# Performance work log

Measured on AMD Instinct MI355X. Metric: run time of the kernel, lower is better.

## Reference

```python
import jax, jax.numpy as jnp
import numpy as np

MARGIN = 1.0
N, D = 4096, 512
NUM_CLASSES = 64


def setup_inputs() -> dict:
    key = jax.random.key(0)
    k1, k2 = jax.random.split(key)
    inputs = jax.random.normal(k1, (N, D), dtype=jnp.float32)
    targets = jax.random.randint(k2, (N,), 0, NUM_CLASSES, dtype=jnp.int64)
    return {"inputs": inputs, "targets": targets}


def reference(inputs, targets):
    n = inputs.shape[0]
    sq = jnp.sum(inputs * inputs, axis=1)  # [n]
    # squared Euclidean distances, clamped at 0 (matches relu in original)
    d2 = jnp.maximum(sq[:, None] + sq[None, :] - 2.0 * (inputs @ inputs.T), 0.0)
    # safe sqrt (zero entries get 0, matching forward; avoids NaN grads)
    dist = jnp.where(d2 > 0, jnp.sqrt(jnp.where(d2 > 0, d2, 1.0)), 0.0)  # [n,n]

    same = targets[:, None] == targets[None, :]
    eye = jnp.eye(n, dtype=bool)
    pos_mask = same & ~eye          # positives, diagonal excluded
    neg_mask = ~same                # negatives (diagonal is same-label, excluded)

    # per-row sum_k exp(margin - d_ik) over negatives  (replaces per-pair loop)
    neg_sum = jnp.sum(jnp.where(neg_mask, jnp.exp(MARGIN - dist), 0.0), axis=1)  # [n]

    # J_ij = log(neg_sum_i + neg_sum_j) + d_ij for positive pairs
    J = jnp.log(neg_sum[:, None] + neg_sum[None, :]) + dist
    triu_pos = jnp.triu(pos_mask)   # loop iterated over upper-triangular positives
    hinge2 = jnp.where(triu_pos, jax.nn.relu(J) ** 2, 0.0)

    # original divides by count of ALL positive entries (both triangles)
    len_p = jnp.sum(pos_mask).astype(jnp.float32)
    return jnp.sum(hinge2) / len_p
```

## Files before the change

kernel.cpp:

```cpp
#include <hip/hip_runtime.h>
#include <math.h>

#define NN 4096
#define DD 512
#define MARGINF 1.0f
#define NCLS 64
#define MAXM 160
#define TRI (MAXM * (MAXM - 1) / 2)

typedef __attribute__((ext_vector_type(8))) short bf16x8;
typedef __attribute__((ext_vector_type(4))) float f32x4;

#define WS_SQ   0
#define WS_NS   4096
#define WS_LOSS 8192
#define WS_CNT  8256
#define WS_RK   8320
#define WS_MEM  12416
#define WS_XB   32768
#define WS_PD   1081344

__device__ __forceinline__ unsigned short f2bf(float f) {
    unsigned u = __float_as_uint(f);
    u += 0x7fffu + ((u >> 16) & 1u);
    return (unsigned short)(u >> 16);
}

__device__ __forceinline__ void gl_lds16(const void* g, void* l) {
    __builtin_amdgcn_global_load_lds(
        (__attribute__((address_space(1))) unsigned int*)g,
        (__attribute__((address_space(3))) unsigned int*)l,
        16, 0, 0);
}

__global__ __launch_bounds__(256) void prep_kernel(const float* __restrict__ X,
                                                   float* __restrict__ ws) {
    const int wv = threadIdx.x >> 6, lane = threadIdx.x & 63;
    const int row = blockIdx.x * 4 + wv;
    const float4* xr = (const float4*)(X + (size_t)row * DD);
    float4 a = xr[lane], b = xr[lane + 64];
    float s = a.x * a.x + a.y * a.y + a.z * a.z + a.w * a.w
            + b.x * b.x + b.y * b.y + b.z * b.z + b.w * b.w;
#pragma unroll
    for (int off = 32; off; off >>= 1) s += __shfl_down(s, off, 64);
    if (lane == 0) { ws[WS_SQ + row] = s; ws[WS_NS + row] = 0.0f; }
    ushort4 pa = {f2bf(a.x), f2bf(a.y), f2bf(a.z), f2bf(a.w)};
    ushort4 pb = {f2bf(b.x), f2bf(b.y), f2bf(b.z), f2bf(b.w)};
    ushort4* xb = (ushort4*)((unsigned short*)(ws + WS_XB) + (size_t)row * DD);
    xb[lane] = pa;
    xb[lane + 64] = pb;
    if (blockIdx.x == 0) {
        if (threadIdx.x < NCLS) ((int*)(ws + WS_CNT))[threadIdx.x] = 0;
        if (threadIdx.x == 0) ws[WS_LOSS] = 0.0f;
    }
}

__global__ __launch_bounds__(256) void class_build_kernel(const int* __restrict__ tgt,
                                                          float* __restrict__ ws) {
    const int t = blockIdx.x * 256 + threadIdx.x;
    const int c = tgt[t];
    int* counts = (int*)(ws + WS_CNT);
    int* rk  = (int*)(ws + WS_RK);
    int* mem = (int*)(ws + WS_MEM);
    int p = atomicAdd(&counts[c], 1);
    rk[t] = p;
    if (p < MAXM) mem[c * MAXM + p] = t;
}

__global__ __launch_bounds__(256) void negsum_kernel(const int* __restrict__ tgt,
                                                     float* __restrict__ ws) {
    __shared__ unsigned short As[128 * 32];
    __shared__ unsigned short Bs[128 * 32];

    const int bidx = blockIdx.x;
    int bj = (int)((sqrtf(8.0f * (float)bidx + 1.0f) - 1.0f) * 0.5f);
    while (bj * (bj + 1) / 2 > bidx) --bj;
    while ((bj + 1) * (bj + 2) / 2 <= bidx) ++bj;
    const int bi = bidx - bj * (bj + 1) / 2;
    const int i0 = bi * 128, j0 = bj * 128;

    const int tid = threadIdx.x;
    const int w = tid >> 6, lane = tid & 63;
    const int lr = lane >> 2, lc = lane & 3;
    const unsigned short* Xb = (const unsigned short*)(ws + WS_XB);

    const unsigned short* ga0 = Xb + (size_t)(i0 + w * 16 + lr) * DD + lc * 8;
    const unsigned short* ga1 = ga0 + (size_t)64 * DD;
    const unsigned short* gb0 = Xb + (size_t)(j0 + w * 16 + lr) * DD + lc * 8;
    const unsigned short* gb1 = gb0 + (size_t)64 * DD;
    unsigned short* la0 = &As[(w * 16) * 32];
    unsigned short* la1 = &As[(64 + w * 16) * 32];
    unsigned short* lb0 = &Bs[(w * 16) * 32];
    unsigned short* lb1 = &Bs[(64 + w * 16) * 32];

    const int m_ = lane & 15, q = lane >> 4;
    const int wrow = (w >> 1) * 64, wcol = (w & 1) * 64;

    f32x4 acc[4][4] = {};

    for (int k0 = 0; k0 < DD; k0 += 32) {
        __syncthreads();
        gl_lds16(ga0 + k0, la0);
        gl_lds16(ga1 + k0, la1);
        gl_lds16(gb0 + k0, lb0);
        gl_lds16(gb1 + k0, lb1);
        __syncthreads();
        bf16x8 af[4], bf[4];
#pragma unroll
        for (int u = 0; u < 4; ++u)
            af[u] = *(const bf16x8*)&As[(wrow + u * 16 + m_) * 32 + q * 8];
#pragma unroll
        for (int v = 0; v < 4; ++v)
            bf[v] = *(const bf16x8*)&Bs[(wcol + v * 16 + m_) * 32 + q * 8];
#pragma unroll
        for (int u = 0; u < 4; ++u)
#pragma unroll
            for (int v = 0; v < 4; ++v)
                acc[u][v] = __builtin_amdgcn_mfma_f32_16x16x32_bf16(
                    af[u], bf[v], acc[u][v], 0, 0, 0);
    }

    const float* sq = ws + WS_SQ;
    float* ns = ws + WS_NS;
    const int* rk = (const int*)(ws + WS_RK);
    float* posd = ws + WS_PD;
    float sjv[4]; int tjv[4], jv[4];
#pragma unroll
    for (int v = 0; v < 4; ++v) {
        int j = j0 + wcol + v * 16 + m_;
        jv[v] = j;
        sjv[v] = sq[j];
        tjv[v] = tgt[j];
    }
    float colp[4] = {0.0f, 0.0f, 0.0f, 0.0f};
#pragma unroll
    for (int u = 0; u < 4; ++u) {
#pragma unroll
        for (int r = 0; r < 4; ++r) {
            const int i = i0 + wrow + u * 16 + q * 4 + r;
            const float si = sq[i];
            const int ti = tgt[i];
            float rp = 0.0f;
#pragma unroll
            for (int v = 0; v < 4; ++v) {
                float d2 = si + sjv[v] - 2.0f * acc[u][v][r];
                float dist = d2 > 0.0f ? sqrtf(d2) : 0.0f;
                if (tjv[v] != ti) {
                    float e = __expf(MARGINF - dist);
                    rp += e;
                    colp[v] += e;
                } else if (i < jv[v]) {
                    int ra = rk[i], rb = rk[jv[v]];
                    if (ra < MAXM && rb < MAXM) {
                        int hi = ra > rb ? ra : rb;
                        int lo = ra > rb ? rb : ra;
                        posd[ti * TRI + hi * (hi - 1) / 2 + lo] = dist;
                    }
                }
            }
            rp += __shfl_xor(rp, 1, 64);
            rp += __shfl_xor(rp, 2, 64);
            rp += __shfl_xor(rp, 4, 64);
            rp += __shfl_xor(rp, 8, 64);
            if (m_ == 0) atomicAdd(&ns[i], rp);
        }
    }
    if (bi != bj) {
#pragma unroll
        for (int v = 0; v < 4; ++v) {
            float cp = colp[v];
            cp += __shfl_xor(cp, 16, 64);
            cp += __shfl_xor(cp, 32, 64);
            if (q == 0) atomicAdd(&ns[jv[v]], cp);
        }
    }
}

__global__ __launch_bounds__(256) void pair2_kernel(float* __restrict__ ws) {
    __shared__ float wsum[4];
    const int c = blockIdx.x;
    int mc = ((const int*)(ws + WS_CNT))[c];
    if (mc > MAXM) mc = MAXM;
    const int P = mc * (mc - 1) / 2;
    const int* mem = (const int*)(ws + WS_MEM) + c * MAXM;
    const float* pd = ws + WS_PD + c * TRI;
    const float* ns = ws + WS_NS;
    float lsum = 0.0f;
    for (int p = threadIdx.x; p < P; p += 256) {
        int b = (int)((1.0f + sqrtf(1.0f + 8.0f * (float)p)) * 0.5f);
        while (b * (b - 1) / 2 > p) --b;
        while ((b + 1) * b / 2 <= p) ++b;
        const int a = p - b * (b - 1) / 2;
        const float dist = pd[b * (b - 1) / 2 + a];
        const int i = mem[a], j = mem[b];
        float J = __logf(ns[i] + ns[j]) + dist;
        float h = fmaxf(J, 0.0f);
        lsum += h * h;
    }
#pragma unroll
    for (int off = 32; off; off >>= 1) lsum += __shfl_xor(lsum, off, 64);
    const int wv = threadIdx.x >> 6, lane = threadIdx.x & 63;
    if (lane == 0) wsum[wv] = lsum;
    __syncthreads();
    if (threadIdx.x == 0) {
        float s = wsum[0] + wsum[1] + wsum[2] + wsum[3];
        if (s != 0.0f) atomicAdd(&ws[WS_LOSS], s);
    }
}

__global__ void finalize_kernel(const float* __restrict__ ws, float* __restrict__ out) {
    const int t = threadIdx.x;
    int mcv = (t < NCLS) ? ((const int*)(ws + WS_CNT))[t] : 0;
    float lp = (float)(mcv * (mcv - 1));
#pragma unroll
    for (int off = 32; off; off >>= 1) lp += __shfl_down(lp, off, 64);
    if (t == 0) out[0] = ws[WS_LOSS] / lp;
}

extern "C" void kernel_launch(void* const* d_in, const int* in_sizes, int n_in,
                              void* d_out, int out_size, void* d_ws, size_t ws_size,
                              hipStream_t stream) {
    const float* X  = (const float*)d_in[0];
    const int*  tgt = (const int*)d_in[1];
    float* ws  = (float*)d_ws;
    float* out = (float*)d_out;

    hipLaunchKernelGGL(prep_kernel, dim3(NN / 4), dim3(256), 0, stream, X, ws);
    hipLaunchKernelGGL(class_build_kernel, dim3(NN / 256), dim3(256), 0, stream, tgt, ws);
    hipLaunchKernelGGL(negsum_kernel, dim3(528), dim3(256), 0, stream, tgt, ws);
    hipLaunchKernelGGL(pair2_kernel, dim3(NCLS), dim3(256), 0, stream, ws);
    hipLaunchKernelGGL(finalize_kernel, dim3(1), dim3(64), 0, stream, ws, out);
}
```

Baseline: 121.7 us.

## Shrink negsum tiles to 64x64 with swizzled LDS layout for more blocks

Changes the distance/negsum GEMM tile from 128x128 to 64x64, so the upper triangle is covered by 2080 blocks instead of 528, and raises the occupancy hint to 8 blocks per CU. It also swizzles the LDS column placement during global-to-LDS loads and fragment reads to reduce bank conflicts. The aim is to fill all CUs on the 256-CU device and cut LDS stalls. The cost is less data reuse per tile, more global/L2 traffic, and more atomics on the row and column sums.

```diff
diff --git a/kernel.cpp b/kernel.cpp
--- a/kernel.cpp
+++ b/kernel.cpp
@@ -7,6 +7,7 @@
 #define NCLS 64
 #define MAXM 160
 #define TRI (MAXM * (MAXM - 1) / 2)
+#define NBLK 2080
 
 typedef __attribute__((ext_vector_type(8))) short bf16x8;
 typedef __attribute__((ext_vector_type(4))) float f32x4;
@@ -59,90 +60,83 @@
                                                           float* __restrict__ ws) {
     const int t = blockIdx.x * 256 + threadIdx.x;
     const int c = tgt[t];
-    int* counts = (int*)(ws + WS_CNT);
-    int* rk  = (int*)(ws + WS_RK);
-    int* mem = (int*)(ws + WS_MEM);
-    int p = atomicAdd(&counts[c], 1);
-    rk[t] = p;
-    if (p < MAXM) mem[c * MAXM + p] = t;
-}
-
-__global__ __launch_bounds__(256) void negsum_kernel(const int* __restrict__ tgt,
-                                                     float* __restrict__ ws) {
-    __shared__ unsigned short As[128 * 32];
-    __shared__ unsigned short Bs[128 * 32];
+    int p = atomicAdd(&((int*)(ws + WS_CNT))[c], 1);
+    ((int*)(ws + WS_RK))[t] = p;
+    if (p < MAXM) ((int*)(ws + WS_MEM))[c * MAXM + p] = t;
+}
+
+__global__ __launch_bounds__(256, 8) void negsum_kernel(const int* __restrict__ tgt,
+                                                        float* __restrict__ ws) {
+    __shared__ unsigned short As[64 * 32];
+    __shared__ unsigned short Bs[64 * 32];
 
     const int bidx = blockIdx.x;
     int bj = (int)((sqrtf(8.0f * (float)bidx + 1.0f) - 1.0f) * 0.5f);
     while (bj * (bj + 1) / 2 > bidx) --bj;
     while ((bj + 1) * (bj + 2) / 2 <= bidx) ++bj;
     const int bi = bidx - bj * (bj + 1) / 2;
-    const int i0 = bi * 128, j0 = bj * 128;
+    const int i0 = bi * 64, j0 = bj * 64;
 
     const int tid = threadIdx.x;
     const int w = tid >> 6, lane = tid & 63;
-    const int lr = lane >> 2, lc = lane & 3;
     const unsigned short* Xb = (const unsigned short*)(ws + WS_XB);
 
-    const unsigned short* ga0 = Xb + (size_t)(i0 + w * 16 + lr) * DD + lc * 8;
-    const unsigned short* ga1 = ga0 + (size_t)64 * DD;
-    const unsigned short* gb0 = Xb + (size_t)(j0 + w * 16 + lr) * DD + lc * 8;
-    const unsigned short* gb1 = gb0 + (size_t)64 * DD;
-    unsigned short* la0 = &As[(w * 16) * 32];
-    unsigned short* la1 = &As[(64 + w * 16) * 32];
-    unsigned short* lb0 = &Bs[(w * 16) * 32];
-    unsigned short* lb1 = &Bs[(64 + w * 16) * 32];
+    const int srow = w * 16 + (lane >> 2);
+    const int sc = (((lane & 3) - (lane >> 3)) & 3) * 8;
+    const unsigned short* gA = Xb + (size_t)(i0 + srow) * DD + sc;
+    const unsigned short* gB = Xb + (size_t)(j0 + srow) * DD + sc;
+    unsigned short* lA = As + w * 512;
+    unsigned short* lB = Bs + w * 512;
 
     const int m_ = lane & 15, q = lane >> 4;
-    const int wrow = (w >> 1) * 64, wcol = (w & 1) * 64;
-
-    f32x4 acc[4][4] = {};
-
-    for (int k0 = 0; k0 < DD; k0 += 32) {
+    const int wr = (w & 1) * 32, wc = (w >> 1) * 32;
+    const int sl = ((q + (m_ >> 1)) & 3) * 8;
+
+    f32x4 acc[2][2] = {};
+
+    for (int it = 0; it < 16; ++it) {
         __syncthreads();
-        gl_lds16(ga0 + k0, la0);
-        gl_lds16(ga1 + k0, la1);
-        gl_lds16(gb0 + k0, lb0);
-        gl_lds16(gb1 + k0, lb1);
+        gl_lds16(gA + it * 32, lA);
+        gl_lds16(gB + it * 32, lB);
         __syncthreads();
-        bf16x8 af[4], bf[4];
-#pragma unroll
-        for (int u = 0; u < 4; ++u)
-            af[u] = *(const bf16x8*)&As[(wrow + u * 16 + m_) * 32 + q * 8];
-#pragma unroll
-        for (int v = 0; v < 4; ++v)
-            bf[v] = *(const bf16x8*)&Bs[(wcol + v * 16 + m_) * 32 + q * 8];
-#pragma unroll
-        for (int u = 0; u < 4; ++u)
-#pragma unroll
-            for (int v = 0; v < 4; ++v)
+        bf16x8 af[2], bfr[2];
+#pragma unroll
+        for (int u = 0; u < 2; ++u)
+            af[u] = *(const bf16x8*)(As + (wr + u * 16 + m_) * 32 + sl);
+#pragma unroll
+        for (int v = 0; v < 2; ++v)
+            bfr[v] = *(const bf16x8*)(Bs + (wc + v * 16 + m_) * 32 + sl);
+#pragma unroll
+        for (int u = 0; u < 2; ++u)
+#pragma unroll
+            for (int v = 0; v < 2; ++v)
                 acc[u][v] = __builtin_amdgcn_mfma_f32_16x16x32_bf16(
-                    af[u], bf[v], acc[u][v], 0, 0, 0);
+                    af[u], bfr[v], acc[u][v], 0, 0, 0);
     }
 
     const float* sq = ws + WS_SQ;
     float* ns = ws + WS_NS;
     const int* rk = (const int*)(ws + WS_RK);
     float* posd = ws + WS_PD;
-    float sjv[4]; int tjv[4], jv[4];
-#pragma unroll
-    for (int v = 0; v < 4; ++v) {
-        int j = j0 + wcol + v * 16 + m_;
+    float sjv[2]; int tjv[2], jv[2];
+#pragma unroll
+    for (int v = 0; v < 2; ++v) {
+        int j = j0 + wc + v * 16 + m_;
         jv[v] = j;
         sjv[v] = sq[j];
         tjv[v] = tgt[j];
     }
-    float colp[4] = {0.0f, 0.0f, 0.0f, 0.0f};
-#pragma unroll
-    for (int u = 0; u < 4; ++u) {
+    float colp[2] = {0.0f, 0.0f};
+#pragma unroll
+    for (int u = 0; u < 2; ++u) {
 #pragma unroll
         for (int r = 0; r < 4; ++r) {
-            const int i = i0 + wrow + u * 16 + q * 4 + r;
+            const int i = i0 + wr + u * 16 + q * 4 + r;
             const float si = sq[i];
             const int ti = tgt[i];
             float rp = 0.0f;
 #pragma unroll
-            for (int v = 0; v < 4; ++v) {
+            for (int v = 0; v < 2; ++v) {
                 float d2 = si + sjv[v] - 2.0f * acc[u][v][r];
                 float dist = d2 > 0.0f ? sqrtf(d2) : 0.0f;
                 if (tjv[v] != ti) {
@@ -167,7 +161,7 @@
     }
     if (bi != bj) {
 #pragma unroll
-        for (int v = 0; v < 4; ++v) {
+        for (int v = 0; v < 2; ++v) {
             float cp = colp[v];
             cp += __shfl_xor(cp, 16, 64);
             cp += __shfl_xor(cp, 32, 64);
@@ -227,7 +221,7 @@
 
     hipLaunchKernelGGL(prep_kernel, dim3(NN / 4), dim3(256), 0, stream, X, ws);
     hipLaunchKernelGGL(class_build_kernel, dim3(NN / 256), dim3(256), 0, stream, tgt, ws);
-    hipLaunchKernelGGL(negsum_kernel, dim3(528), dim3(256), 0, stream, tgt, ws);
+    hipLaunchKernelGGL(negsum_kernel, dim3(NBLK), dim3(256), 0, stream, tgt, ws);
     hipLaunchKernelGGL(pair2_kernel, dim3(NCLS), dim3(256), 0, stream, ws);
     hipLaunchKernelGGL(finalize_kernel, dim3(1), dim3(64), 0, stream, ws, out);
 }
```

Measured after the change: 119.7 us. Within noise of the previous version (-1.7%).
